# Performance work log

Hardware: AMD Instinct MI355X
Metric: run time of the kernel (lower is better)

Reference implementation:

```python
import jax, jax.numpy as jnp
import numpy as np
import math

B, S, D = 2, 1024, 2048
NH, NKV, HD = 16, 8, 128
NREP = NH // NKV
WINDOW = 256  # = max_seq_len; ReRoPE window


def _rope(x, cos, sin):
    # x: (b, s, h, d); cos/sin broadcastable to (b, s, h, d//2). Interleaved pairs (llama2.c style).
    b, s, h, d = x.shape
    xr, xi = x[..., ::2], x[..., 1::2]
    or_ = xr * cos - xi * sin
    oi = xr * sin + xi * cos
    return jnp.stack([or_, oi], axis=-1).reshape(b, s, h, d)


def setup_inputs() -> dict:
    key = jax.random.key(0)
    kx, kq, kk, kv, ko = jax.random.split(key, 5)
    # real RoPE tables (theta=10000), per-position, half head dim
    inv = 1.0 / (10000.0 ** (np.arange(0, HD, 2, dtype=np.float32) / HD))
    fr = np.outer(np.arange(S, dtype=np.float32), inv).astype(np.float32)  # (S, HD//2)
    sc = 0.02
    return {
        "x": jax.random.normal(kx, (B, S, D), jnp.float32),
        "freqs_cos": jnp.asarray(np.cos(fr)),
        "freqs_sin": jnp.asarray(np.sin(fr)),
        "wq": jax.random.normal(kq, (D, NH * HD), jnp.float32) * sc,
        "wk": jax.random.normal(kk, (D, NKV * HD), jnp.float32) * sc,
        "wv": jax.random.normal(kv, (D, NKV * HD), jnp.float32) * sc,
        "wo": jax.random.normal(ko, (NH * HD, D), jnp.float32) * sc,
    }


def reference(x, freqs_cos, freqs_sin, wq, wk, wv, wo):
    b, s, _ = x.shape
    xq = (x @ wq).reshape(b, s, NH, HD)
    xk = (x @ wk).reshape(b, s, NKV, HD)
    xv = (x @ wv).reshape(b, s, NKV, HD)

    cos = freqs_cos[:s][None, :, None, :]
    sin = freqs_sin[:s][None, :, None, :]
    q1 = _rope(xq, cos, sin)   # standard RoPE
    k1 = _rope(xk, cos, sin)

    # ReRoPE: queries rotated at the fixed clamp position = window; keys unrotated
    cw = freqs_cos[WINDOW][None, None, None, :]
    sw = freqs_sin[WINDOW][None, None, None, :]
    q2 = _rope(xq, cw, sw)
    k2 = xk

    rep = lambda a: jnp.repeat(a, NREP, axis=2)          # repeat_kv (GQA)
    heads = lambda a: a.transpose(0, 2, 1, 3)            # (b, h, s, d)
    q1, k1, v = heads(q1), heads(rep(k1)), heads(rep(xv))
    q2, k2 = heads(q2), heads(rep(k2))

    scale = 1.0 / math.sqrt(HD)
    s1 = jnp.einsum("bhqd,bhkd->bhqk", q1, k1) * scale
    s2 = jnp.einsum("bhqd,bhkd->bhqk", q2, k2) * scale

    i = jnp.arange(s)[:, None]
    j = jnp.arange(s)[None, :]
    causal = j <= i
    rect = causal & (j > i - WINDOW)                     # rectified_mask band
    scores = jnp.where(rect, s1, s2)
    scores = jnp.where(causal, scores, -jnp.inf)         # mask_inf (causal)

    attn = jax.nn.softmax(scores.astype(jnp.float32), axis=-1).astype(x.dtype)
    out = jnp.einsum("bhqk,bhkd->bhqd", attn, v)
    out = out.transpose(0, 2, 1, 3).reshape(b, s, NH * HD)
    return out @ wo
```

## Files before the change

### kernel.cpp

```cpp
#include <hip/hip_runtime.h>
#include <hip/hip_bf16.h>

#define BDIM 2
#define SDIM 1024
#define DDIM 2048
#define NH 16
#define NKV 8
#define HD 128
#define WINDOW 256

typedef __bf16 bf16;
typedef __bf16 bf16x4 __attribute__((ext_vector_type(4)));
typedef __bf16 bf16x8 __attribute__((ext_vector_type(8)));
typedef float f32x4 __attribute__((ext_vector_type(4)));

#define L2E 1.44269504088896341f

__device__ inline bf16x8 load8(const bf16* p) { return *reinterpret_cast<const bf16x8*>(p); }

__device__ __forceinline__ void gl_lds16(const bf16* g, bf16* l) {
  __builtin_amdgcn_global_load_lds(
      (__attribute__((address_space(1))) void*)g,
      (__attribute__((address_space(3))) void*)l,
      16, 0, 0);
}

__global__ __launch_bounds__(256) void prep(const float* __restrict__ x,
                                            const float* __restrict__ wq,
                                            const float* __restrict__ wk,
                                            const float* __restrict__ wv,
                                            const float* __restrict__ wo,
                                            bf16* __restrict__ xb,
                                            bf16* __restrict__ wqkvT,
                                            bf16* __restrict__ woT) {
  __shared__ bf16 tl[64][72];
  int z = blockIdx.z;
  int t = threadIdx.x;
  if (z == 4) {
    long base = ((long)(blockIdx.y * 32 + blockIdx.x)) * 4096;
    const float* xs = x + base;
    bf16* xo = xb + base;
#pragma unroll
    for (int e = 0; e < 4; ++e) {
      float4 a = *(const float4*)&xs[(e * 256 + t) * 4];
      bf16x4 o;
      o[0] = (bf16)a.x; o[1] = (bf16)a.y; o[2] = (bf16)a.z; o[3] = (bf16)a.w;
      *(bf16x4*)&xo[(e * 256 + t) * 4] = o;
    }
    return;
  }
  const float* src; bf16* dst; int C;
  if (z == 0)      { src = wq; dst = wqkvT;                 C = 2048; }
  else if (z == 1) { src = wk; dst = wqkvT + 2048L * 2048;  C = 1024; }
  else if (z == 2) { src = wv; dst = wqkvT + 3072L * 2048;  C = 1024; }
  else             { src = wo; dst = woT;                   C = 2048; }
  int c0 = blockIdx.x * 64, r0 = blockIdx.y * 64;
  if (c0 >= C) return;
  int tx = t & 15, ty = t >> 4;
#pragma unroll
  for (int rr = 0; rr < 4; ++rr) {
    int row = ty + rr * 16;
    float4 a = *(const float4*)&src[(long)(r0 + row) * C + c0 + tx * 4];
    bf16x4 o;
    o[0] = (bf16)a.x; o[1] = (bf16)a.y; o[2] = (bf16)a.z; o[3] = (bf16)a.w;
    *(bf16x4*)&tl[row][tx * 4] = o;
  }
  __syncthreads();
#pragma unroll
  for (int rr = 0; rr < 4; ++rr) {
    int cc = ty + rr * 16;
    bf16x4 o;
#pragma unroll
    for (int e = 0; e < 4; ++e) o[e] = tl[tx * 4 + e][cc];
    *(bf16x4*)&dst[(long)(c0 + cc) * 2048 + r0 + tx * 4] = o;
  }
}

__global__ __launch_bounds__(512) void gemm_bt128(const bf16* __restrict__ A,
                                                  const bf16* __restrict__ Bt,
                                                  float* __restrict__ C,
                                                  int M, int N, int K) {
  __shared__ bf16 smem[2 * 16384];
  int t = threadIdx.x;
  int wid = t >> 6, lane = t & 63;
  int wm = (wid >> 2) * 64, wn = (wid & 3) * 32;
  int fm = lane & 15, quad = lane >> 4;

  int wg = blockIdx.y * 16 + blockIdx.x;
  int swz = (wg & 7) * 32 + (wg >> 3);
  int by = swz >> 4, bx = swz & 15;
  int m0 = by * 128, n0 = bx * 128;

  const bf16* Ag = A + (long)m0 * K;
  const bf16* Bg = Bt + (long)n0 * K;

  f32x4 acc[4][2] = {};

  auto stA = [&](bf16* dst, int k0, int p) {
    int idx = p * 512 + t;
    int row = idx >> 3, ccs = idx & 7;
    int gcol = ((ccs ^ (row & 7)) * 8);
    gl_lds16(&Ag[(long)row * K + k0 + gcol], &dst[idx * 8]);
  };
  auto stB = [&](bf16* dst, int k0, int p) {
    int idx = p * 512 + t;
    int row = idx >> 3, ccs = idx & 7;
    int gcol = ((ccs ^ (row & 7)) * 8);
    gl_lds16(&Bg[(long)row * K + k0 + gcol], &dst[idx * 8]);
  };
  auto cmp = [&](const bf16* As, const bf16* Bs, int ks) {
    int cc = (ks >> 3) + quad;
    bf16x8 af[4], bfr[2];
    for (int i = 0; i < 4; ++i) {
      int fr = wm + i * 16 + fm;
      af[i] = load8(&As[(fr * 8 + (cc ^ (fr & 7))) * 8]);
    }
    for (int j = 0; j < 2; ++j) {
      int fr = wn + j * 16 + fm;
      bfr[j] = load8(&Bs[(fr * 8 + (cc ^ (fr & 7))) * 8]);
    }
    __builtin_amdgcn_s_setprio(1);
    for (int i = 0; i < 4; ++i)
      for (int j = 0; j < 2; ++j)
        acc[i][j] = __builtin_amdgcn_mfma_f32_16x16x32_bf16(af[i], bfr[j], acc[i][j], 0, 0, 0);
    __builtin_amdgcn_s_setprio(0);
  };

  {
    bf16* As = smem; bf16* Bs = smem + 8192;
    stA(As, 0, 0); stA(As, 0, 1);
    stB(Bs, 0, 0); stB(Bs, 0, 1);
  }
  const int NT = K / 64;
  for (int kt = 0; kt < NT; ++kt) {
    int cur = kt & 1;
    bf16* As = smem + cur * 16384;
    bf16* Bs = As + 8192;
    if (kt + 1 < NT) {
      bf16* An = smem + (cur ^ 1) * 16384;
      bf16* Bn = An + 8192;
      int kn = (kt + 1) * 64;
      stA(An, kn, 0); stB(Bn, kn, 0);
      asm volatile("s_waitcnt vmcnt(2)\n\ts_barrier" ::: "memory");
      cmp(As, Bs, 0);
      stA(An, kn, 1); stB(Bn, kn, 1);
      cmp(As, Bs, 32);
      asm volatile("s_barrier" ::: "memory");
    } else {
      asm volatile("s_waitcnt vmcnt(0)\n\ts_barrier" ::: "memory");
      cmp(As, Bs, 0);
      cmp(As, Bs, 32);
    }
  }
  for (int i = 0; i < 4; ++i)
    for (int r = 0; r < 4; ++r) {
      int row = m0 + wm + i * 16 + quad * 4 + r;
      for (int j = 0; j < 2; ++j) {
        int col = n0 + wn + j * 16 + fm;
        C[(long)row * N + col] = acc[i][j][r];
      }
    }
}

#define VPITCH 130
__global__ __launch_bounds__(512) void gemm_qkv(const bf16* __restrict__ A,
                                                const bf16* __restrict__ Bt,
                                                const float* __restrict__ fc,
                                                const float* __restrict__ fs,
                                                bf16* __restrict__ q0,
                                                bf16* __restrict__ k1,
                                                bf16* __restrict__ k2,
                                                bf16* __restrict__ vT) {
  const int K = 2048;
  __shared__ bf16 smem[2 * 24576];
  int t = threadIdx.x;
  int wid = t >> 6, lane = t & 63;
  int wm = (wid >> 2) * 64, wn = (wid & 3) * 64;
  int fm = lane & 15, quad = lane >> 4;

  int wg = blockIdx.y * 16 + blockIdx.x;
  int swz = (wg & 7) * 32 + (wg >> 3);
  int by = swz >> 4, bx = swz & 15;
  int m0 = by * 128, n0 = bx * 256;

  const bf16* Ag = A + (long)m0 * K;
  const bf16* Bg = Bt + (long)n0 * K;

  f32x4 acc[4][4] = {};

  auto stA = [&](bf16* dst, int k0, int p) {
    int idx = p * 512 + t;
    int row = idx >> 3, ccs = idx & 7;
    int gcol = ((ccs ^ (row & 7)) * 8);
    gl_lds16(&Ag[(long)row * K + k0 + gcol], &dst[idx * 8]);
  };
  auto stB = [&](bf16* dst, int k0, int p) {
    int idx = p * 512 + t;
    int row = idx >> 3, ccs = idx & 7;
    int gcol = ((ccs ^ (row & 7)) * 8);
    gl_lds16(&Bg[(long)row * K + k0 + gcol], &dst[idx * 8]);
  };
  auto cmp = [&](const bf16* As, const bf16* Bs, int ks) {
    int cc = (ks >> 3) + quad;
    bf16x8 af[4], bfr[4];
    for (int i = 0; i < 4; ++i) {
      int fr = wm + i * 16 + fm;
      af[i] = load8(&As[(fr * 8 + (cc ^ (fr & 7))) * 8]);
    }
    for (int j = 0; j < 4; ++j) {
      int fr = wn + j * 16 + fm;
      bfr[j] = load8(&Bs[(fr * 8 + (cc ^ (fr & 7))) * 8]);
    }
    __builtin_amdgcn_s_setprio(1);
    for (int i = 0; i < 4; ++i)
      for (int j = 0; j < 4; ++j)
        acc[i][j] = __builtin_amdgcn_mfma_f32_16x16x32_bf16(af[i], bfr[j], acc[i][j], 0, 0, 0);
    __builtin_amdgcn_s_setprio(0);
  };

  {
    bf16* As = smem; bf16* Bs = smem + 8192;
    stA(As, 0, 0); stA(As, 0, 1);
    stB(Bs, 0, 0); stB(Bs, 0, 1); stB(Bs, 0, 2); stB(Bs, 0, 3);
  }
  const int NT = K / 64;
  for (int kt = 0; kt < NT; ++kt) {
    int cur = kt & 1;
    bf16* As = smem + cur * 24576;
    bf16* Bs = As + 8192;
    if (kt + 1 < NT) {
      bf16* An = smem + (cur ^ 1) * 24576;
      bf16* Bn = An + 8192;
      int kn = (kt + 1) * 64;
      stA(An, kn, 0); stA(An, kn, 1); stB(Bn, kn, 0);
      asm volatile("s_waitcnt vmcnt(3)\n\ts_barrier" ::: "memory");
      cmp(As, Bs, 0);
      stB(Bn, kn, 1); stB(Bn, kn, 2); stB(Bn, kn, 3);
      cmp(As, Bs, 32);
      asm volatile("s_barrier" ::: "memory");
    } else {
      asm volatile("s_waitcnt vmcnt(0)\n\ts_barrier" ::: "memory");
      cmp(As, Bs, 0);
      cmp(As, Bs, 32);
    }
  }

  if (n0 < 2048) {
    const float scale = 0.08838834764831845f;
    for (int i = 0; i < 4; ++i)
      for (int r = 0; r < 4; ++r) {
        int row = m0 + wm + i * 16 + quad * 4 + r;
        for (int j = 0; j < 4; ++j) {
          int gc = n0 + wn + j * 16 + fm;
          q0[(long)row * 2048 + gc] = (bf16)(acc[i][j][r] * scale);
        }
      }
  } else if (n0 < 3072) {
    float sgn = (lane & 1) ? 1.f : -1.f;
    float cwj[4], swj[4];
    for (int j = 0; j < 4; ++j) {
      int dp = ((wn + j * 16 + fm) & 127) >> 1;
      cwj[j] = fc[WINDOW * 64 + dp];
      swj[j] = fs[WINDOW * 64 + dp] * (-sgn);
    }
    for (int i = 0; i < 4; ++i)
      for (int r = 0; r < 4; ++r) {
        int row = m0 + wm + i * 16 + quad * 4 + r;
        int s = row & (SDIM - 1);
        for (int j = 0; j < 4; ++j) {
          int kc = n0 - 2048 + wn + j * 16 + fm;
          int dp = (kc & 127) >> 1;
          float v = acc[i][j][r];
          float pp = __shfl_xor(v, 1, 64);
          float c = fc[s * 64 + dp];
          float sn = fs[s * 64 + dp] * sgn;
          long dst = (long)row * 1024 + kc;
          k1[dst] = (bf16)(v * c + pp * sn);
          k2[dst] = (bf16)(v * cwj[j] + pp * swj[j]);
        }
      }
  } else {
    int vv0 = (n0 - 3072) >> 7;
    int s0l = m0 & (SDIM - 1);
    int bq = m0 >> 10;
    for (int half = 0; half < 2; ++half) {
      __syncthreads();
      if (((wn >> 7) & 1) == half) {
        for (int i = 0; i < 4; ++i)
          for (int j = 0; j < 4; ++j) {
            int col = (wn & 127) + j * 16 + fm;
            for (int r = 0; r < 4; ++r) {
              int rl = wm + i * 16 + quad * 4 + r;
              smem[col * VPITCH + rl] = (bf16)acc[i][j][r];
            }
          }
      }
      __syncthreads();
      bf16* vtg = vT + ((long)(bq * NKV + vv0 + half)) * 128 * 1024;
      for (int p = 0; p < 4; ++p) {
        int c = p * 512 + t;
        int d = c >> 4, sc = (c & 15) * 8;
        *(bf16x8*)&vtg[(long)d * 1024 + s0l + sc] = *(bf16x8*)&smem[d * VPITCH + sc];
      }
    }
  }
}

__global__ __launch_bounds__(256) void attn_kernel(const bf16* __restrict__ q0,
                                                   const bf16* __restrict__ k1,
                                                   const bf16* __restrict__ k2,
                                                   const bf16* __restrict__ vT,
                                                   const float* __restrict__ fc,
                                                   const float* __restrict__ fs,
                                                   bf16* __restrict__ aout) {
  __shared__ bf16 Kb[2][8192];
  __shared__ bf16 Vb[2][8192];
  __shared__ bf16 Pl[4][16][72];
  __shared__ float stats[4][16];

  int h = blockIdx.y;
  int b = blockIdx.z;
  int tile = b ? (15 - blockIdx.x) : blockIdx.x;
  int kv = h >> 1;
  int t = threadIdx.x;
  int w = t >> 6, lane = t & 63;
  int m = lane & 15, quad = lane >> 4;

  const bf16* k1g0 = k1 + ((long)b * SDIM) * 1024 + kv * 128;
  const bf16* k2g0 = k2 + ((long)b * SDIM) * 1024 + kv * 128;
  const bf16* vtg0 = vT + ((long)(b * NKV + kv)) * 128 * 1024;

  int t0 = tile * 64;
  int i0w = t0 + w * 16;

  const bf16* q0p = q0 + ((long)(b * SDIM + i0w + m)) * 2048 + h * 128 + quad * 8;
  bf16x8 q0f[4], q1f[4];
  int srow = i0w + m;
  for (int kc = 0; kc < 4; ++kc) {
    q0f[kc] = load8(q0p + kc * 32);
    for (int p4 = 0; p4 < 4; ++p4) {
      int dp = kc * 16 + quad * 4 + p4;
      float c = fc[srow * 64 + dp], sn = fs[srow * 64 + dp];
      float xr = (float)q0f[kc][2 * p4], xi = (float)q0f[kc][2 * p4 + 1];
      q1f[kc][2 * p4]     = (bf16)(xr * c - xi * sn);
      q1f[kc][2 * p4 + 1] = (bf16)(xr * sn + xi * c);
    }
  }

  int NS2 = tile >= 4 ? tile - 3 : 0;
  int NSEG = NS2 + (tile < 4 ? tile + 1 : 5);
  int j1base = tile >= 4 ? t0 - 256 : 0;

  auto stage = [&](int s) {
    int j0, md;
    if (s < NS2) { j0 = s * 64; md = 2; } else { j0 = j1base + (s - NS2) * 64; md = 1; }
    const bf16* kg0 = (md == 1) ? k1g0 : k2g0;
    bf16* Kd = Kb[s & 1];
    bf16* Vd = Vb[s & 1];
    for (int p = 0; p < 4; ++p) {
      int idx = p * 256 + t;
      int kr = idx >> 4, kcs = idx & 15;
      int kg = (kcs ^ (kr & 15)) * 8;
      gl_lds16(&kg0[(long)(j0 + kr) * 1024 + kg], &Kd[idx * 8]);
      int vd = idx >> 3, vcs = idx & 7;
      int vg = (vcs ^ (vd & 7)) * 8;
      gl_lds16(&vtg0[(long)vd * 1024 + j0 + vg], &Vd[idx * 8]);
    }
  };

  f32x4 o[8] = {};
  float mrow = -30.f, lrow = 0.f;
  int i = i0w + m;

  stage(0);
  for (int s = 0; s < NSEG; ++s) {
    if (s + 1 < NSEG) {
      stage(s + 1);
      asm volatile("s_waitcnt vmcnt(8)\n\ts_barrier" ::: "memory");
    } else {
      asm volatile("s_waitcnt vmcnt(0)\n\ts_barrier" ::: "memory");
    }
    int j0, md;
    if (s < NS2) { j0 = s * 64; md = 2; } else { j0 = j1base + (s - NS2) * 64; md = 1; }
    bool fullseg = (md == 2) ? (s < NS2 - 1)
                             : (j0 >= t0 - 192 && j0 <= t0 - 64);
    const bf16* Ks = Kb[s & 1];
    const bf16* VTs = Vb[s & 1];

    f32x4 sc[4] = {};
    if (md == 1) {
      for (int st = 0; st < 4; ++st)
        for (int kc = 0; kc < 4; ++kc) {
          int cc = kc * 4 + quad;
          sc[st] = __builtin_amdgcn_mfma_f32_16x16x32_bf16(
              load8(&Ks[((st * 16 + m) * 16 + (cc ^ m)) * 8]), q1f[kc], sc[st], 0, 0, 0);
        }
    } else {
      for (int st = 0; st < 4; ++st)
        for (int kc = 0; kc < 4; ++kc) {
          int cc = kc * 4 + quad;
          sc[st] = __builtin_amdgcn_mfma_f32_16x16x32_bf16(
              load8(&Ks[((st * 16 + m) * 16 + (cc ^ m)) * 8]), q0f[kc], sc[st], 0, 0, 0);
        }
    }

    float sv[4][4];
    for (int st = 0; st < 4; ++st)
      for (int r = 0; r < 4; ++r) {
        float v = sc[st][r];
        if (!fullseg) {
          int j = j0 + st * 16 + quad * 4 + r;
          if (md == 1) {
            if (j > i || j <= i - WINDOW) v = -INFINITY;
          } else {
            if (j > i - WINDOW) v = -INFINITY;
          }
        }
        sv[st][r] = v;
      }

    float pv[4][4];
    for (int st = 0; st < 4; ++st)
      for (int r = 0; r < 4; ++r)
        pv[st][r] = exp2f((sv[st][r] - mrow) * L2E);
    float bm = -INFINITY;
    for (int st = 0; st < 4; ++st)
      for (int r = 0; r < 4; ++r) bm = fmaxf(bm, sv[st][r]);
    bm = fmaxf(bm, __shfl_xor(bm, 16, 64));
    bm = fmaxf(bm, __shfl_xor(bm, 32, 64));
    if (!__all(bm <= mrow + 8.f)) {
      float mnew = fmaxf(mrow, bm);
      float alpha = exp2f((mrow - mnew) * L2E);
      for (int st = 0; st < 4; ++st)
        for (int r = 0; r < 4; ++r) pv[st][r] *= alpha;
      lrow *= alpha;
      if (lane < 16) stats[w][lane] = alpha;
      f32x4 av = *(f32x4*)&stats[w][quad * 4];
      for (int n8 = 0; n8 < 8; ++n8)
        for (int r = 0; r < 4; ++r) o[n8][r] *= av[r];
      mrow = mnew;
    }
    float rs = 0.f;
    for (int st = 0; st < 4; ++st) {
      bf16x4 pk;
      for (int r = 0; r < 4; ++r) {
        rs += pv[st][r];
        pk[r] = (bf16)pv[st][r];
      }
      *(bf16x4*)&Pl[w][m][st * 16 + quad * 4] = pk;
    }
    rs += __shfl_xor(rs, 16, 64);
    rs += __shfl_xor(rs, 32, 64);
    lrow += rs;

    for (int kc = 0; kc < 2; ++kc) {
      bf16x8 af = load8(&Pl[w][m][kc * 32 + quad * 8]);
      int cc = kc * 4 + quad;
      for (int n8 = 0; n8 < 8; ++n8) {
        int d = n8 * 16 + m;
        o[n8] = __builtin_amdgcn_mfma_f32_16x16x32_bf16(
            af, load8(&VTs[(d * 8 + (cc ^ (d & 7))) * 8]), o[n8], 0, 0, 0);
      }
    }
    asm volatile("s_barrier" ::: "memory");
  }

  if (lane < 16) stats[w][lane] = lrow;
  __builtin_amdgcn_s_waitcnt(0);
  f32x4 lv = *(f32x4*)&stats[w][quad * 4];
  for (int n8 = 0; n8 < 8; ++n8)
    for (int r = 0; r < 4; ++r) {
      int row = i0w + quad * 4 + r;
      float val = o[n8][r] / lv[r];
      aout[((long)(b * SDIM + row)) * 2048 + h * 128 + n8 * 16 + m] = (bf16)val;
    }
}

extern "C" void kernel_launch(void* const* d_in, const int* in_sizes, int n_in,
                              void* d_out, int out_size, void* d_ws, size_t ws_size,
                              hipStream_t stream) {
  const float* x  = (const float*)d_in[0];
  const float* fc = (const float*)d_in[1];
  const float* fs = (const float*)d_in[2];
  const float* wq = (const float*)d_in[3];
  const float* wk = (const float*)d_in[4];
  const float* wv = (const float*)d_in[5];
  const float* wo = (const float*)d_in[6];
  float* out = (float*)d_out;

  bf16* wqkvT = (bf16*)d_ws;
  bf16* woT   = wqkvT + 4096L * 2048;
  bf16* xb    = woT + 2048L * 2048;
  bf16* q0b   = xb + 2048L * 2048;
  bf16* k1b   = q0b + 2048L * 2048;
  bf16* k2b   = k1b + 2048L * 1024;
  bf16* vT    = k2b + 2048L * 1024;
  bf16* aout  = vT + 2048L * 1024;

  prep<<<dim3(32, 32, 5), 256, 0, stream>>>(x, wq, wk, wv, wo, xb, wqkvT, woT);

  gemm_qkv<<<dim3(16, 16), 512, 0, stream>>>(xb, wqkvT, fc, fs, q0b, k1b, k2b, vT);

  attn_kernel<<<dim3(16, 16, 2), 256, 0, stream>>>(q0b, k1b, k2b, vT, fc, fs, aout);

  gemm_bt128<<<dim3(16, 16), 512, 0, stream>>>(aout, woT, out, 2048, 2048, 2048);
}
```

Before: 220.7 us.

## Triple-buffer QKV GEMM LDS stages with two-tile prefetch depth

Changes the QKV projection GEMM from a double-buffered LDS pipeline with split loads to a three-stage ring buffer that prefetches two k-tiles ahead, with one barrier per iteration. The goal is to hide global-to-LDS load latency better and remove the second barrier per iteration. The cost is that LDS use grows from 96KB to 144KB per block, which may reduce occupancy. The vmcnt(6) count must match the six loads issued per stage.

Measured after the change: 216.8 us. Within noise of the previous version (-1.8%).

```diff
diff --git a/kernel.cpp b/kernel.cpp
--- a/kernel.cpp
+++ b/kernel.cpp
@@ -172,7 +172,7 @@
                                                 bf16* __restrict__ k2,
                                                 bf16* __restrict__ vT) {
   const int K = 2048;
-  __shared__ bf16 smem[2 * 24576];
+  __shared__ bf16 smem[3 * 24576];
   int t = threadIdx.x;
   int wid = t >> 6, lane = t & 63;
   int wm = (wid >> 2) * 64, wn = (wid & 3) * 64;
@@ -188,17 +188,24 @@
 
   f32x4 acc[4][4] = {};
 
-  auto stA = [&](bf16* dst, int k0, int p) {
-    int idx = p * 512 + t;
-    int row = idx >> 3, ccs = idx & 7;
-    int gcol = ((ccs ^ (row & 7)) * 8);
-    gl_lds16(&Ag[(long)row * K + k0 + gcol], &dst[idx * 8]);
-  };
-  auto stB = [&](bf16* dst, int k0, int p) {
-    int idx = p * 512 + t;
-    int row = idx >> 3, ccs = idx & 7;
-    int gcol = ((ccs ^ (row & 7)) * 8);
-    gl_lds16(&Bg[(long)row * K + k0 + gcol], &dst[idx * 8]);
+  auto stage = [&](int kt) {
+    bf16* As = smem + (kt % 3) * 24576;
+    bf16* Bs = As + 8192;
+    int k0 = kt * 64;
+    {
+      int idx = t;
+      int row = idx >> 3, ccs = idx & 7;
+      gl_lds16(&Ag[(long)row * K + k0 + ((ccs ^ (row & 7)) * 8)], &As[idx * 8]);
+      idx = 512 + t;
+      row = idx >> 3; ccs = idx & 7;
+      gl_lds16(&Ag[(long)row * K + k0 + ((ccs ^ (row & 7)) * 8)], &As[idx * 8]);
+    }
+#pragma unroll
+    for (int p = 0; p < 4; ++p) {
+      int idx = p * 512 + t;
+      int row = idx >> 3, ccs = idx & 7;
+      gl_lds16(&Bg[(long)row * K + k0 + ((ccs ^ (row & 7)) * 8)], &Bs[idx * 8]);
+    }
   };
   auto cmp = [&](const bf16* As, const bf16* Bs, int ks) {
     int cc = (ks >> 3) + quad;
@@ -218,31 +225,21 @@
     __builtin_amdgcn_s_setprio(0);
   };
 
-  {
-    bf16* As = smem; bf16* Bs = smem + 8192;
-    stA(As, 0, 0); stA(As, 0, 1);
-    stB(Bs, 0, 0); stB(Bs, 0, 1); stB(Bs, 0, 2); stB(Bs, 0, 3);
-  }
   const int NT = K / 64;
+  stage(0);
+  stage(1);
   for (int kt = 0; kt < NT; ++kt) {
-    int cur = kt & 1;
-    bf16* As = smem + cur * 24576;
+    if (kt + 1 < NT) {
+      asm volatile("s_waitcnt vmcnt(6)" ::: "memory");
+    } else {
+      asm volatile("s_waitcnt vmcnt(0)" ::: "memory");
+    }
+    __builtin_amdgcn_s_barrier();
+    if (kt + 2 < NT) stage(kt + 2);
+    bf16* As = smem + (kt % 3) * 24576;
     bf16* Bs = As + 8192;
-    if (kt + 1 < NT) {
-      bf16* An = smem + (cur ^ 1) * 24576;
-      bf16* Bn = An + 8192;
-      int kn = (kt + 1) * 64;
-      stA(An, kn, 0); stA(An, kn, 1); stB(Bn, kn, 0);
-      asm volatile("s_waitcnt vmcnt(3)\n\ts_barrier" ::: "memory");
-      cmp(As, Bs, 0);
-      stB(Bn, kn, 1); stB(Bn, kn, 2); stB(Bn, kn, 3);
-      cmp(As, Bs, 32);
-      asm volatile("s_barrier" ::: "memory");
-    } else {
-      asm volatile("s_waitcnt vmcnt(0)\n\ts_barrier" ::: "memory");
-      cmp(As, Bs, 0);
-      cmp(As, Bs, 32);
-    }
+    cmp(As, Bs, 0);
+    cmp(As, Bs, 32);
   }
 
   if (n0 < 2048) {
```
